# Optimization experiments

Hardware: AMD Instinct MI355X
Metric: run time of the kernel (lower is better)

## Reference

```python
import jax, jax.numpy as jnp
import numpy as np

T, B, N, L = 1024, 2, 10000, 30   # frames, batch(=2, hardcoded in original), vocab, glosses/sample
S = 2 * L + 1                      # blank-interleaved (CTC-extended) label length


def setup_inputs() -> dict:
    key = jax.random.key(0)
    k1, k2 = jax.random.split(key)
    logits = jax.random.normal(k1, (T, B, N), dtype=jnp.float32)
    label = jax.random.randint(k2, (B * L,), 1, N, dtype=jnp.int32)  # real glosses are >=1 (0 is blank)
    logits_len = jnp.full((B,), T, dtype=jnp.int32)
    label_len = jnp.full((B,), L, dtype=jnp.int32)
    return {"logits": logits, "logits_len": logits_len, "label": label, "label_len": label_len}


def _extend(lab):
    # [l1, l2, ...] -> [0, l1, 0, l2, ..., 0]  (blank-interleaved), shape (S,)
    return jnp.zeros((S,), lab.dtype).at[1::2].set(lab)


def _reach_fwd(ext):
    # map_forward[j, i] > 0  <=>  state j reachable from start at time i (CTC forward lattice).
    pad2 = jnp.full((2,), -1, ext.dtype)
    allow2 = (ext != 0) & (ext != jnp.concatenate([pad2, ext[:-2]]))  # skip-2 allowed
    init = jnp.zeros((S,), bool).at[0].set(True).at[1].set(True)

    def step(c, _):
        s1 = jnp.concatenate([jnp.zeros((1,), bool), c[:-1]])
        s2 = jnp.concatenate([jnp.zeros((2,), bool), c[:-2]]) & allow2
        n = c | s1 | s2
        return n, n

    _, outs = jax.lax.scan(step, init, None, length=T - 1)
    return jnp.concatenate([init[None], outs], axis=0)  # (T, S)


def _reach_bwd(ext):
    # map_backward[j, i] > 0  <=>  end reachable from state j at time i.
    pad2 = jnp.full((2,), -1, ext.dtype)
    allow2 = (ext != 0) & (ext != jnp.concatenate([ext[2:], pad2]))
    init = jnp.zeros((S,), bool).at[S - 1].set(True).at[S - 2].set(True)

    def step(c, _):
        s1 = jnp.concatenate([c[1:], jnp.zeros((1,), bool)])
        s2 = jnp.concatenate([c[2:], jnp.zeros((2,), bool)]) & allow2
        n = c | s1 | s2
        return n, n

    _, outs = jax.lax.scan(step, init, None, length=T - 1)
    return jnp.concatenate([outs[::-1], init[None]], axis=0)  # (T, S), time 0..T-1


def _forward(logits, label):
    labels = label.reshape(B, L)
    ext = jax.vmap(_extend)(labels)            # (B, S)
    rf = jax.vmap(_reach_fwd)(ext)             # (B, T, S)
    rb = jax.vmap(_reach_bwd)(ext)             # (B, T, S)
    sel = (rf & rb).astype(logits.dtype)       # map_final != 0 on the lattice

    def per_sample(logit, e, s):
        # mask[t, v] = any lattice state j with ext[j] == v active at time t
        mask = jnp.zeros((T, N), logit.dtype).at[:, e].max(s) > 0
        # original builds final_label as a detached numpy copy of logit at masked entries
        target = jax.lax.stop_gradient(jnp.where(mask, logit, jnp.zeros((), logit.dtype)))
        return jnp.sum((logit - target) ** 2)  # nn.MSELoss(reduction='sum')

    losses = jax.vmap(per_sample)(jnp.transpose(logits, (1, 0, 2)), ext, sel)
    return jnp.mean(losses)  # (loss1 + loss2) / 2


def reference(logits, logits_len, label, label_len):
    # logits_len / label_len are fixed to full lengths (T, L) so shapes stay static.
    return _forward(logits, label)
```

## Files before the change

kernel.cpp:

```cpp
#include <hip/hip_runtime.h>
#include <stdint.h>

typedef unsigned long long u64;

static constexpr int T = 1024;
static constexpr int B = 2;
static constexpr int N = 10000;
static constexpr int L = 30;
static constexpr int S = 2 * L + 1;

static constexpr int NBLK  = 2048;
static constexpr int CHUNK = 2500;
static constexpr int TAIL  = CHUNK - 9 * 256;

static constexpr u64 ALL   = (1ULL << S) - 1;
static constexpr u64 EVENM = 0x5555555555555555ULL & ((1ULL << S) - 1);

__device__ __forceinline__ float block_reduce(float s) {
    for (int off = 32; off; off >>= 1) s += __shfl_down(s, off, 64);
    __shared__ float tmp[8];
    int lane = threadIdx.x & 63, w = threadIdx.x >> 6;
    int nw = blockDim.x >> 6;
    if (lane == 0) tmp[w] = s;
    __syncthreads();
    float t = 0.f;
    if (threadIdx.x == 0)
        for (int i = 0; i < nw; ++i) t += tmp[i];
    return t;
}

__device__ __forceinline__ float sq4(float4 v) {
    return v.x * v.x + v.y * v.y + v.z * v.z + v.w * v.w;
}

__global__ void k_fused(const float4* __restrict__ x4, const float* __restrict__ x,
                        const int* __restrict__ label, float* __restrict__ partials) {
    float s = 0.f;
    int tid = threadIdx.x;

    if (blockIdx.x < 256) {
        __shared__ int labs[B][L];
        __shared__ u64 dups[B][L];
        __shared__ u64 AfS[B], AbS[B];
        if (tid < B) {
            int b = tid;
            int lb[L];
            u64 Af = 0, Ab = 0;
            #pragma unroll
            for (int k = 0; k < L; ++k) { lb[k] = label[b * L + k]; labs[b][k] = lb[k]; }
            #pragma unroll
            for (int k = 0; k < L; ++k) {
                u64 bit = 1ULL << (2 * k + 1);
                if (k == 0     || lb[k] != lb[k - 1]) Af |= bit;
                if (k == L - 1 || lb[k] != lb[k + 1]) Ab |= bit;
                u64 d = 0;
                for (int k2 = 0; k2 < k; ++k2)
                    if (lb[k2] == lb[k]) d |= 1ULL << (2 * k2 + 1);
                dups[b][k] = d;
            }
            AfS[b] = Af; AbS[b] = Ab;
        }
        __syncthreads();
        int pair = blockIdx.x * 8 + (tid >> 5);
        int lane = tid & 31;
        int b = pair >> 10;
        int t = pair & (T - 1);
        u64 m;
        if (t < 64) {
            u64 Af = AfS[b];
            u64 c = 3ULL;
            for (int i = 0; i < t; ++i) c = (c | (c << 1) | ((c << 2) & Af)) & ALL;
            m = c;
        } else if (t >= T - 64) {
            u64 Ab = AbS[b];
            u64 c = (1ULL << (S - 1)) | (1ULL << (S - 2));
            int n = T - 1 - t;
            for (int i = 0; i < n; ++i) c = c | (c >> 1) | ((c >> 2) & Ab);
            m = c;
        } else {
            m = ALL;
        }
        const float* row = x + (size_t)t * (B * N) + (size_t)b * N;
        if (lane < L) {
            u64 bit = 1ULL << (2 * lane + 1);
            if ((m & bit) && !(m & dups[b][lane])) {
                float v = row[labs[b][lane]];
                s -= v * v;
            }
        } else if (lane == L) {
            if (m & EVENM) { float v = row[0]; s -= v * v; }
        }
    }

    const float4* p = x4 + (size_t)blockIdx.x * CHUNK + tid;
    float4 v[5];
    #pragma unroll
    for (int j = 0; j < 5; ++j) v[j] = p[j * 256];
    #pragma unroll
    for (int j = 0; j < 5; ++j) s += sq4(v[j]);
    #pragma unroll
    for (int j = 0; j < 4; ++j) v[j] = p[(5 + j) * 256];
    v[4] = (tid < TAIL) ? p[9 * 256] : make_float4(0.f, 0.f, 0.f, 0.f);
    #pragma unroll
    for (int j = 0; j < 5; ++j) s += sq4(v[j]);

    float tot = block_reduce(s);
    if (threadIdx.x == 0) partials[blockIdx.x] = tot;
}

__global__ void k_final(const float* __restrict__ partials, float* __restrict__ out) {
    float s = 0.f;
    for (int i = threadIdx.x; i < NBLK; i += 256) s += partials[i];
    float tot = block_reduce(s);
    if (threadIdx.x == 0) out[0] = 0.5f * tot;
}

extern "C" void kernel_launch(void* const* d_in, const int* in_sizes, int n_in,
                              void* d_out, int out_size, void* d_ws, size_t ws_size,
                              hipStream_t stream) {
    const float* logits = (const float*)d_in[0];
    const int*   label  = (const int*)d_in[2];
    float* partials = (float*)d_ws;

    k_fused<<<NBLK, 256, 0, stream>>>((const float4*)logits, logits, label, partials);
    k_final<<<1, 256, 0, stream>>>(partials, (float*)d_out);
}
```

Before: 119.2 us.

## Spread CTC lattice correction across all blocks using wave shuffles

Before, the first 256 blocks each rebuilt the label bitmasks with only two threads, running a serial O(L^2) duplicate scan followed by a __syncthreads, and each handled 8 (b,t) pairs. Now every block handles exactly one (b,t) pair. Its first 32 lanes build the skip and duplicate masks in parallel by broadcasting labels with __shfl, so the shared-memory staging and its barrier are gone. The first five float4 loads of the sum-of-squares stream are issued before this correction work so memory latency overlaps with it. The cost is that the mask-building and reachability loops are now repeated in every block instead of once per group of eight pairs.

```diff
diff --git a/kernel.cpp b/kernel.cpp
--- a/kernel.cpp
+++ b/kernel.cpp
@@ -18,14 +18,13 @@
 
 __device__ __forceinline__ float block_reduce(float s) {
     for (int off = 32; off; off >>= 1) s += __shfl_down(s, off, 64);
-    __shared__ float tmp[8];
+    __shared__ float tmp[4];
     int lane = threadIdx.x & 63, w = threadIdx.x >> 6;
-    int nw = blockDim.x >> 6;
     if (lane == 0) tmp[w] = s;
     __syncthreads();
     float t = 0.f;
     if (threadIdx.x == 0)
-        for (int i = 0; i < nw; ++i) t += tmp[i];
+        for (int i = 0; i < 4; ++i) t += tmp[i];
     return t;
 }
 
@@ -35,44 +34,45 @@
 
 __global__ void k_fused(const float4* __restrict__ x4, const float* __restrict__ x,
                         const int* __restrict__ label, float* __restrict__ partials) {
+    int tid = threadIdx.x;
     float s = 0.f;
-    int tid = threadIdx.x;
 
-    if (blockIdx.x < 256) {
-        __shared__ int labs[B][L];
-        __shared__ u64 dups[B][L];
-        __shared__ u64 AfS[B], AbS[B];
-        if (tid < B) {
-            int b = tid;
-            int lb[L];
-            u64 Af = 0, Ab = 0;
-            #pragma unroll
-            for (int k = 0; k < L; ++k) { lb[k] = label[b * L + k]; labs[b][k] = lb[k]; }
-            #pragma unroll
-            for (int k = 0; k < L; ++k) {
-                u64 bit = 1ULL << (2 * k + 1);
-                if (k == 0     || lb[k] != lb[k - 1]) Af |= bit;
-                if (k == L - 1 || lb[k] != lb[k + 1]) Ab |= bit;
-                u64 d = 0;
-                for (int k2 = 0; k2 < k; ++k2)
-                    if (lb[k2] == lb[k]) d |= 1ULL << (2 * k2 + 1);
-                dups[b][k] = d;
+    const float4* p = x4 + (size_t)blockIdx.x * CHUNK + tid;
+    float4 v0 = p[0 * 256];
+    float4 v1 = p[1 * 256];
+    float4 v2 = p[2 * 256];
+    float4 v3 = p[3 * 256];
+    float4 v4 = p[4 * 256];
+
+    if (tid < 32) {
+        int lane = tid;
+        int b = blockIdx.x >> 10;
+        int t = blockIdx.x & (T - 1);
+        int myl = (lane < L) ? label[b * L + lane] : 0;
+
+        u64 Af = 0, Ab = 0, dup = 0;
+        int prev = -1;
+        #pragma unroll
+        for (int k2 = 0; k2 < L; ++k2) {
+            int lk = __shfl(myl, k2, 64);
+            u64 bitk = 1ULL << (2 * k2 + 1);
+            if (k2 == 0) {
+                Af |= bitk;
+            } else if (lk != prev) {
+                Af |= bitk;
+                Ab |= 1ULL << (2 * (k2 - 1) + 1);
             }
-            AfS[b] = Af; AbS[b] = Ab;
+            if (lk == myl && k2 < lane) dup |= bitk;
+            prev = lk;
         }
-        __syncthreads();
-        int pair = blockIdx.x * 8 + (tid >> 5);
-        int lane = tid & 31;
-        int b = pair >> 10;
-        int t = pair & (T - 1);
+        Ab |= 1ULL << (2 * (L - 1) + 1);
+
         u64 m;
         if (t < 64) {
-            u64 Af = AfS[b];
             u64 c = 3ULL;
             for (int i = 0; i < t; ++i) c = (c | (c << 1) | ((c << 2) & Af)) & ALL;
             m = c;
         } else if (t >= T - 64) {
-            u64 Ab = AbS[b];
             u64 c = (1ULL << (S - 1)) | (1ULL << (S - 2));
             int n = T - 1 - t;
             for (int i = 0; i < n; ++i) c = c | (c >> 1) | ((c >> 2) & Ab);
@@ -80,29 +80,26 @@
         } else {
             m = ALL;
         }
+
         const float* row = x + (size_t)t * (B * N) + (size_t)b * N;
         if (lane < L) {
             u64 bit = 1ULL << (2 * lane + 1);
-            if ((m & bit) && !(m & dups[b][lane])) {
-                float v = row[labs[b][lane]];
-                s -= v * v;
+            if ((m & bit) && !(m & dup)) {
+                float vv = row[myl];
+                s -= vv * vv;
             }
         } else if (lane == L) {
-            if (m & EVENM) { float v = row[0]; s -= v * v; }
+            if (m & EVENM) { float vv = row[0]; s -= vv * vv; }
         }
     }
 
-    const float4* p = x4 + (size_t)blockIdx.x * CHUNK + tid;
-    float4 v[5];
-    #pragma unroll
-    for (int j = 0; j < 5; ++j) v[j] = p[j * 256];
-    #pragma unroll
-    for (int j = 0; j < 5; ++j) s += sq4(v[j]);
-    #pragma unroll
-    for (int j = 0; j < 4; ++j) v[j] = p[(5 + j) * 256];
-    v[4] = (tid < TAIL) ? p[9 * 256] : make_float4(0.f, 0.f, 0.f, 0.f);
-    #pragma unroll
-    for (int j = 0; j < 5; ++j) s += sq4(v[j]);
+    s += sq4(v0); s += sq4(v1); s += sq4(v2); s += sq4(v3); s += sq4(v4);
+    v0 = p[5 * 256];
+    v1 = p[6 * 256];
+    v2 = p[7 * 256];
+    v3 = p[8 * 256];
+    v4 = (tid < TAIL) ? p[9 * 256] : make_float4(0.f, 0.f, 0.f, 0.f);
+    s += sq4(v0); s += sq4(v1); s += sq4(v2); s += sq4(v3); s += sq4(v4);
 
     float tot = block_reduce(s);
     if (threadIdx.x == 0) partials[blockIdx.x] = tot;
```

New measurement: 122.4 us. 1.03x slower.
